# Kernel tuning notes

Hardware: AMD Instinct MI355X
Metric: run time of the kernel (lower is better)

## Reference

```python
import jax, jax.numpy as jnp
import numpy as np

N_HEADS = 16


def setup_inputs() -> dict:
    key = jax.random.key(0)
    ks = jax.random.split(key, 9)
    B, S, D = 2, 2048, 1024
    sc = 0.02
    return {
        'x': jax.random.normal(ks[0], (B, S, D), jnp.float32),
        'Wq': jax.random.normal(ks[1], (D, D), jnp.float32) * sc,
        'bq': jax.random.normal(ks[2], (D,), jnp.float32) * sc,
        'Wk': jax.random.normal(ks[3], (D, D), jnp.float32) * sc,
        'bk': jax.random.normal(ks[4], (D,), jnp.float32) * sc,
        'Wv': jax.random.normal(ks[5], (D, D), jnp.float32) * sc,
        'bv': jax.random.normal(ks[6], (D,), jnp.float32) * sc,
        'Wo': jax.random.normal(ks[7], (D, D), jnp.float32) * sc,
        'bo': jax.random.normal(ks[8], (D,), jnp.float32) * sc,
    }


def reference(x, Wq, bq, Wk, bk, Wv, bv, Wo, bo):
    # Chunked causal prefill. The chunk-wise mask (q_pos >= kv_pos over the
    # growing KV cache) is mathematically identical to full causal attention,
    # so we compute it as one vectorized masked softmax attention.
    B, S, D = x.shape
    H = N_HEADS
    hd = D // H

    def proj(W, b):
        # torch Linear: y = x @ W.T + b ; then split heads -> [B,H,S,hd]
        y = jnp.einsum('bsd,ed->bse', x, W) + b
        return y.reshape(B, S, H, hd).transpose(0, 2, 1, 3)

    q = proj(Wq, bq)
    k = proj(Wk, bk)
    v = proj(Wv, bv)

    scores = jnp.einsum('bhqd,bhkd->bhqk', q, k) / jnp.sqrt(jnp.asarray(hd, x.dtype))
    causal = jnp.tril(jnp.ones((S, S), dtype=bool))  # [S,S]
    scores = jnp.where(causal[None, None], scores, jnp.asarray(-jnp.inf, scores.dtype))
    attn = jax.nn.softmax(scores, axis=-1)
    ctx = jnp.einsum('bhqk,bhkd->bhqd', attn, v)  # [B,H,S,hd]
    ctx = ctx.transpose(0, 2, 1, 3).reshape(B, S, D)
    out = jnp.einsum('bsd,ed->bse', ctx, Wo) + bo
    return out
```

## Files before the change

### kernel.cpp

```cpp
#include <hip/hip_runtime.h>
#include <cstdint>
#include <math.h>

typedef _Float16 f16;
typedef _Float16 f16x2 __attribute__((ext_vector_type(2)));
typedef _Float16 f16x4 __attribute__((ext_vector_type(4)));
typedef _Float16 f16x8 __attribute__((ext_vector_type(8)));
typedef __fp16   h16x2 __attribute__((ext_vector_type(2)));
typedef float    f32x4 __attribute__((ext_vector_type(4)));

__device__ __forceinline__ f32x4 mfma16(f16x8 a, f16x8 b, f32x4 c) {
  return __builtin_amdgcn_mfma_f32_16x16x32_f16(a, b, c, 0, 0, 0);
}
__device__ __forceinline__ void gl2lds16(const f16* g, f16* l) {
  __builtin_amdgcn_global_load_lds((__attribute__((address_space(1))) void*)(g),
                                   (__attribute__((address_space(3))) void*)(l),
                                   16, 0, 0);
}
__device__ __forceinline__ float fexp2(float x) { return __builtin_amdgcn_exp2f(x); }
__device__ __forceinline__ f16x2 pkrtz(float a, float b) {
  h16x2 r = __builtin_amdgcn_cvt_pkrtz(a, b);
  return __builtin_bit_cast(f16x2, r);
}
__device__ __forceinline__ float dot2acc(f16x2 a, f16x2 b, float c) {
#if __has_builtin(__builtin_amdgcn_fdot2)
  return __builtin_amdgcn_fdot2(__builtin_bit_cast(h16x2, a),
                                __builtin_bit_cast(h16x2, b), c, false);
#else
  return c + (float)a[0] * (float)b[0] + (float)a[1] * (float)b[1];
#endif
}

__global__ __launch_bounds__(256) void cvt_kernel(
    const float* __restrict__ x,  const float* __restrict__ wq, const float* __restrict__ wk,
    const float* __restrict__ wv, const float* __restrict__ wo,
    f16* __restrict__ xh, f16* __restrict__ wqkvh, f16* __restrict__ woh)
{
  const int seg = blockIdx.y;
  const float* src; f16* dst; int n;
  if      (seg == 0) { src = x;  dst = xh;              n = 4194304; }
  else if (seg == 1) { src = wq; dst = wqkvh;           n = 1048576; }
  else if (seg == 2) { src = wk; dst = wqkvh + 1048576; n = 1048576; }
  else if (seg == 3) { src = wv; dst = wqkvh + 2097152; n = 1048576; }
  else               { src = wo; dst = woh;             n = 1048576; }
  const int idx = (int)(blockIdx.x * 256 + threadIdx.x) * 8;
  if (idx >= n) return;
  f32x4 a = *(const f32x4*)(src + idx);
  f32x4 b = *(const f32x4*)(src + idx + 4);
  f16x8 h;
  h[0] = (f16)a[0]; h[1] = (f16)a[1]; h[2] = (f16)a[2]; h[3] = (f16)a[3];
  h[4] = (f16)b[0]; h[5] = (f16)b[1]; h[6] = (f16)b[2]; h[7] = (f16)b[3];
  *(f16x8*)(dst + idx) = h;
}

__global__ __launch_bounds__(256) void gemm_qkv(
    const f16* __restrict__ A, const f16* __restrict__ B,
    const float* __restrict__ bias0, const float* __restrict__ bias1, const float* __restrict__ bias2,
    f16* __restrict__ Qp, f16* __restrict__ Kp, f16* __restrict__ Vp)
{
  constexpr int K = 1024;
  __shared__ __align__(16) f16 As[128 * 32];
  __shared__ __align__(16) f16 Bs[128 * 32];
  const int tid  = threadIdx.x;
  const int wave = tid >> 6, lane = tid & 63;
  const int quad = lane >> 4, col = lane & 15;
  const int tile_m = blockIdx.y * 128, tile_n = blockIdx.x * 128;
  const int mb = (wave >> 1) * 64, nb = (wave & 1) * 64;
  const int srow = lane >> 2, scol = (lane & 3) * 8;
  const f16* gA = A + (size_t)(tile_m + wave * 32 + srow) * K + scol;
  const f16* gB = B + (size_t)(tile_n + wave * 32 + srow) * K + scol;
  f16* lA = As + wave * 1024;
  f16* lB = Bs + wave * 1024;

  f32x4 acc[4][4] = {};
  for (int k0 = 0; k0 < K; k0 += 32) {
    gl2lds16(gA + k0,          lA);
    gl2lds16(gA + 16 * K + k0, lA + 512);
    gl2lds16(gB + k0,          lB);
    gl2lds16(gB + 16 * K + k0, lB + 512);
    __syncthreads();
    f16x8 af[4], bf[4];
    #pragma unroll
    for (int i = 0; i < 4; ++i)
      af[i] = *(const f16x8*)&As[(mb + i * 16 + col) * 32 + quad * 8];
    #pragma unroll
    for (int j = 0; j < 4; ++j)
      bf[j] = *(const f16x8*)&Bs[(nb + j * 16 + col) * 32 + quad * 8];
    #pragma unroll
    for (int i = 0; i < 4; ++i)
      #pragma unroll
      for (int j = 0; j < 4; ++j)
        acc[i][j] = mfma16(af[i], bf[j], acc[i][j]);
    __syncthreads();
  }

  #pragma unroll
  for (int j = 0; j < 4; ++j) {
    const int gn = tile_n + nb + j * 16 + col;
    const int which = gn >> 10;
    const int d = gn & 1023;
    const float* bp = (which == 0) ? bias0 : (which == 1) ? bias1 : bias2;
    f16* dst        = (which == 0) ? Qp    : (which == 1) ? Kp    : Vp;
    const float bvv = bp[d];
    const float qs  = (which == 0) ? 0.18033688f : 1.0f;
    const int h = d >> 6, hi = d & 63;
    #pragma unroll
    for (int i = 0; i < 4; ++i) {
      #pragma unroll
      for (int r = 0; r < 4; ++r) {
        const int gm = tile_m + mb + i * 16 + quad * 4 + r;
        const int bb = gm >> 11, s = gm & 2047;
        dst[(((size_t)bb * 16 + h) * 2048 + s) * 64 + hi] = (f16)((acc[i][j][r] + bvv) * qs);
      }
    }
  }
}

__global__ __launch_bounds__(256) void vtrans_kernel(
    const f16* __restrict__ Vh, f16* __restrict__ Vt)
{
  __shared__ __align__(16) f16 t[64][72];
  const int bh = blockIdx.y;
  const int s0 = blockIdx.x * 64;
  const int tid = threadIdx.x;
  const int sr = tid >> 2, dc = (tid & 3) * 16;
  const size_t ib = ((size_t)bh * 2048 + s0 + sr) * 64 + dc;
  f16x8 v0 = *(const f16x8*)&Vh[ib];
  f16x8 v1 = *(const f16x8*)&Vh[ib + 8];
  *(f16x8*)&t[sr][dc]     = v0;
  *(f16x8*)&t[sr][dc + 8] = v1;
  __syncthreads();
  const int d = tid >> 2, sc = (tid & 3) * 16;
  f16x8 o0, o1;
  #pragma unroll
  for (int j = 0; j < 8; ++j) { o0[j] = t[sc + j][d]; o1[j] = t[sc + 8 + j][d]; }
  const size_t ob = ((size_t)bh * 64 + d) * 2048 + s0 + sc;
  *(f16x8*)&Vt[ob]     = o0;
  *(f16x8*)&Vt[ob + 8] = o1;
}

__global__ __launch_bounds__(256) void attn_kernel(
    const f16* __restrict__ Q, const f16* __restrict__ K, const f16* __restrict__ Vt,
    f16* __restrict__ ctx)
{
  __shared__ __align__(16) f16 Ks[2][64 * 72];
  __shared__ __align__(16) f16 Vts[2][64 * 72];
  __shared__ __align__(16) f16 Ps[4][16 * 72];

  const int bh  = blockIdx.x;
  const int tid = threadIdx.x;
  const int wave = tid >> 6, lane = tid & 63;
  const int quad = lane >> 4, col = lane & 15;
  const int b = bh >> 4, h = bh & 15;
  const size_t base = (size_t)bh * 2048 * 64;
  const size_t vtb  = (size_t)bh * 64 * 2048;

  int srow[2], sc8[2];
  #pragma unroll
  for (int i = 0; i < 2; ++i) {
    const int flat = tid + i * 256;
    srow[i] = flat >> 3;
    sc8[i]  = (flat & 7) * 8;
  }

  auto run_tile = [&](int qt) {
    const int q0 = qt * 64;
    const int qa = q0 + wave * 16;
    const f16x8 bqa0 = *(const f16x8*)&Q[base + (size_t)(qa + col) * 64 + quad * 8];
    const f16x8 bqa1 = *(const f16x8*)&Q[base + (size_t)(qa + col) * 64 + 32 + quad * 8];

    f32x4 cta[4] = {};
    float ma = -INFINITY;
    float la = 0.f;

    f16x8 kr[2], vr[2];
    auto gload = [&](int t) {
      #pragma unroll
      for (int i = 0; i < 2; ++i) {
        kr[i] = *(const f16x8*)&K[base + (size_t)(t * 64 + srow[i]) * 64 + sc8[i]];
        vr[i] = *(const f16x8*)&Vt[vtb + (size_t)srow[i] * 2048 + t * 64 + sc8[i]];
      }
    };
    auto swrite = [&](int buf) {
      #pragma unroll
      for (int i = 0; i < 2; ++i) {
        *(f16x8*)&Ks[buf][srow[i] * 72 + sc8[i]]  = kr[i];
        *(f16x8*)&Vts[buf][srow[i] * 72 + sc8[i]] = vr[i];
      }
    };

    const int nIter = qt + 1;

    gload(0);
    __syncthreads();
    swrite(0);
    if (nIter > 1) gload(1);

    for (int t = 0; t < nIter; ++t) {
      const int cur = t & 1;
      __syncthreads();
      if (t + 1 < nIter) {
        swrite(cur ^ 1);
        if (t + 2 < nIter) gload(t + 2);
      }

      f32x4 sa[4];
      #pragma unroll
      for (int jt = 0; jt < 4; ++jt) {
        const int kro = (jt * 16 + col) * 72;
        const f16x8 ak0 = *(const f16x8*)&Ks[cur][kro + quad * 8];
        const f16x8 ak1 = *(const f16x8*)&Ks[cur][kro + 32 + quad * 8];
        f32x4 za = {};
        za = mfma16(ak0, bqa0, za);
        sa[jt] = mfma16(ak1, bqa1, za);
      }

      if (t == qt) {
        #pragma unroll
        for (int jt = 0; jt < 4; ++jt) {
          const int kg = t * 64 + jt * 16 + quad * 4;
          #pragma unroll
          for (int r = 0; r < 4; ++r) {
            if (kg + r > qa + col) sa[jt][r] = -1e30f;
          }
        }
      }

      float tm = fmaxf(fmaxf(sa[0][0], sa[0][1]), fmaxf(sa[0][2], sa[0][3]));
      #pragma unroll
      for (int jt = 1; jt < 4; ++jt)
        tm = fmaxf(tm, fmaxf(fmaxf(sa[jt][0], sa[jt][1]), fmaxf(sa[jt][2], sa[jt][3])));
      tm = fmaxf(tm, __shfl_xor(tm, 16));
      tm = fmaxf(tm, __shfl_xor(tm, 32));

      if (__any(tm > ma + 6.f)) {
        const float mnew = fmaxf(ma, tm);
        const float alpha = fexp2(ma - mnew);
        ma = mnew;
        la *= alpha;
        f32x4 ava;
        #pragma unroll
        for (int r = 0; r < 4; ++r) ava[r] = __shfl(alpha, quad * 4 + r);
        #pragma unroll
        for (int jd = 0; jd < 4; ++jd) cta[jd] *= ava;
      }

      const f16x2 one2 = {(_Float16)1.f, (_Float16)1.f};
      float rs = 0.f;
      #pragma unroll
      for (int jt = 0; jt < 4; ++jt) {
        const f16x2 a01 = pkrtz(fexp2(sa[jt][0] - ma), fexp2(sa[jt][1] - ma));
        const f16x2 a23 = pkrtz(fexp2(sa[jt][2] - ma), fexp2(sa[jt][3] - ma));
        rs = dot2acc(a01, one2, rs);
        rs = dot2acc(a23, one2, rs);
        f16x4 pw; pw[0] = a01[0]; pw[1] = a01[1]; pw[2] = a23[0]; pw[3] = a23[1];
        *(f16x4*)&Ps[wave][col * 72 + jt * 16 + quad * 4] = pw;
      }
      la += rs;

      __asm__ volatile("s_waitcnt lgkmcnt(0)" ::: "memory");

      const f16x8 apa0 = *(const f16x8*)&Ps[wave][col * 72 + quad * 8];
      const f16x8 apa1 = *(const f16x8*)&Ps[wave][col * 72 + 32 + quad * 8];
      #pragma unroll
      for (int jd = 0; jd < 4; ++jd) {
        const int vro = (jd * 16 + col) * 72;
        const f16x8 bv0 = *(const f16x8*)&Vts[cur][vro + quad * 8];
        const f16x8 bv1 = *(const f16x8*)&Vts[cur][vro + 32 + quad * 8];
        cta[jd] = mfma16(apa1, bv1, mfma16(apa0, bv0, cta[jd]));
      }
    }

    la += __shfl_xor(la, 16);
    la += __shfl_xor(la, 32);
    f32x4 lva;
    #pragma unroll
    for (int r = 0; r < 4; ++r) lva[r] = __shfl(la, quad * 4 + r);
    #pragma unroll
    for (int jd = 0; jd < 4; ++jd) {
      #pragma unroll
      for (int r = 0; r < 4; ++r) {
        const int qga = qa + quad * 4 + r;
        const int d = h * 64 + jd * 16 + col;
        ctx[((size_t)b * 2048 + qga) * 1024 + d] = (f16)(cta[jd][r] / lva[r]);
      }
    }
  };

  run_tile(blockIdx.y);
  run_tile(31 - blockIdx.y);
}

__global__ __launch_bounds__(256) void gemm_o(
    const f16* __restrict__ A, const f16* __restrict__ B, const float* __restrict__ bias,
    float* __restrict__ Out)
{
  constexpr int K = 1024;
  __shared__ __align__(16) f16 As[128 * 32];
  __shared__ __align__(16) f16 Bs[64 * 32];
  const int tid  = threadIdx.x;
  const int wave = tid >> 6, lane = tid & 63;
  const int quad = lane >> 4, col = lane & 15;
  const int tile_m = blockIdx.y * 128, tile_n = blockIdx.x * 64;
  const int mb = wave * 32;
  const int srow = lane >> 2, scol = (lane & 3) * 8;
  const f16* gA = A + (size_t)(tile_m + wave * 32 + srow) * K + scol;
  const f16* gB = B + (size_t)(tile_n + wave * 16 + srow) * K + scol;
  f16* lA = As + wave * 1024;
  f16* lB = Bs + wave * 512;

  f32x4 acc[2][4] = {};
  for (int k0 = 0; k0 < K; k0 += 32) {
    gl2lds16(gA + k0,          lA);
    gl2lds16(gA + 16 * K + k0, lA + 512);
    gl2lds16(gB + k0,          lB);
    __syncthreads();
    f16x8 af[2], bf[4];
    #pragma unroll
    for (int i = 0; i < 2; ++i)
      af[i] = *(const f16x8*)&As[(mb + i * 16 + col) * 32 + quad * 8];
    #pragma unroll
    for (int j = 0; j < 4; ++j)
      bf[j] = *(const f16x8*)&Bs[(j * 16 + col) * 32 + quad * 8];
    #pragma unroll
    for (int i = 0; i < 2; ++i)
      #pragma unroll
      for (int j = 0; j < 4; ++j)
        acc[i][j] = mfma16(af[i], bf[j], acc[i][j]);
    __syncthreads();
  }

  #pragma unroll
  for (int j = 0; j < 4; ++j) {
    const int gn = tile_n + j * 16 + col;
    const float bvv = bias[gn];
    #pragma unroll
    for (int i = 0; i < 2; ++i) {
      #pragma unroll
      for (int r = 0; r < 4; ++r) {
        const int gm = tile_m + mb + i * 16 + quad * 4 + r;
        Out[(size_t)gm * 1024 + gn] = acc[i][j][r] + bvv;
      }
    }
  }
}

extern "C" void kernel_launch(void* const* d_in, const int* in_sizes, int n_in,
                              void* d_out, int out_size, void* d_ws, size_t ws_size,
                              hipStream_t stream)
{
  const float* x  = (const float*)d_in[0];
  const float* Wq = (const float*)d_in[1];
  const float* bq = (const float*)d_in[2];
  const float* Wk = (const float*)d_in[3];
  const float* bk = (const float*)d_in[4];
  const float* Wv = (const float*)d_in[5];
  const float* bv = (const float*)d_in[6];
  const float* Wo = (const float*)d_in[7];
  const float* bo = (const float*)d_in[8];
  float* out = (float*)d_out;

  f16* ws = (f16*)d_ws;
  const size_t M1 = 1048576;
  f16* xh    = ws;
  f16* wqkvh = ws + 4  * M1;
  f16* woh   = ws + 7  * M1;
  f16* Qh    = ws + 8  * M1;
  f16* Kh    = ws + 12 * M1;
  f16* Vh    = ws + 16 * M1;
  f16* Vth   = ws + 20 * M1;
  f16* ctxh  = ws + 24 * M1;

  cvt_kernel<<<dim3(2048, 5), 256, 0, stream>>>(x, Wq, Wk, Wv, Wo, xh, wqkvh, woh);
  gemm_qkv<<<dim3(24, 32), 256, 0, stream>>>(xh, wqkvh, bq, bk, bv, Qh, Kh, Vh);
  vtrans_kernel<<<dim3(32, 32), 256, 0, stream>>>(Vh, Vth);
  attn_kernel<<<dim3(32, 16), 256, 0, stream>>>(Qh, Kh, Vth, ctxh);
  gemm_o<<<dim3(16, 32), 256, 0, stream>>>(ctxh, woh, bo, out);
}
```

Baseline: 191.6 us.

## Fuse paired causal query tiles into one KV sweep sharing K/V loads

Instead of running the short and long query tiles one after another, each block now streams KV tiles once for the long tile and also computes the short tile while its causal range is active. K/V tiles staged in shared memory are reused by both query tiles, which roughly halves global K/V traffic and barrier count per block. The blockIdx.y to tile-pair mapping is changed and occupancy is hinted with launch_bounds(256,4). The cost is more registers for two accumulator sets and a branchy loop body, which could limit occupancy or cause spills.

```diff
diff --git a/kernel.cpp b/kernel.cpp
--- a/kernel.cpp
+++ b/kernel.cpp
@@ -139,15 +139,18 @@
   *(f16x8*)&Vt[ob + 8] = o1;
 }
 
-__global__ __launch_bounds__(256) void attn_kernel(
+__global__ __launch_bounds__(256, 4) void attn_kernel(
     const f16* __restrict__ Q, const f16* __restrict__ K, const f16* __restrict__ Vt,
     f16* __restrict__ ctx)
 {
   __shared__ __align__(16) f16 Ks[2][64 * 72];
   __shared__ __align__(16) f16 Vts[2][64 * 72];
-  __shared__ __align__(16) f16 Ps[4][16 * 72];
+  __shared__ __align__(16) f16 Ps[4][2][16 * 72];
 
   const int bh  = blockIdx.x;
+  const int yy  = blockIdx.y;
+  const int p   = (yy < 8) ? yy : 23 - yy;
+  const int qlong = 31 - p, qshort = p;
   const int tid = threadIdx.x;
   const int wave = tid >> 6, lane = tid & 63;
   const int quad = lane >> 4, col = lane & 15;
@@ -163,76 +166,93 @@
     sc8[i]  = (flat & 7) * 8;
   }
 
-  auto run_tile = [&](int qt) {
-    const int q0 = qt * 64;
-    const int qa = q0 + wave * 16;
-    const f16x8 bqa0 = *(const f16x8*)&Q[base + (size_t)(qa + col) * 64 + quad * 8];
-    const f16x8 bqa1 = *(const f16x8*)&Q[base + (size_t)(qa + col) * 64 + 32 + quad * 8];
-
-    f32x4 cta[4] = {};
-    float ma = -INFINITY;
-    float la = 0.f;
-
-    f16x8 kr[2], vr[2];
-    auto gload = [&](int t) {
-      #pragma unroll
-      for (int i = 0; i < 2; ++i) {
-        kr[i] = *(const f16x8*)&K[base + (size_t)(t * 64 + srow[i]) * 64 + sc8[i]];
-        vr[i] = *(const f16x8*)&Vt[vtb + (size_t)srow[i] * 2048 + t * 64 + sc8[i]];
-      }
-    };
-    auto swrite = [&](int buf) {
-      #pragma unroll
-      for (int i = 0; i < 2; ++i) {
-        *(f16x8*)&Ks[buf][srow[i] * 72 + sc8[i]]  = kr[i];
-        *(f16x8*)&Vts[buf][srow[i] * 72 + sc8[i]] = vr[i];
-      }
-    };
-
-    const int nIter = qt + 1;
-
-    gload(0);
+  const int qa = qlong * 64 + wave * 16;
+  const int qb = qshort * 64 + wave * 16;
+  const f16x8 bqa0 = *(const f16x8*)&Q[base + (size_t)(qa + col) * 64 + quad * 8];
+  const f16x8 bqa1 = *(const f16x8*)&Q[base + (size_t)(qa + col) * 64 + 32 + quad * 8];
+  const f16x8 bqb0 = *(const f16x8*)&Q[base + (size_t)(qb + col) * 64 + quad * 8];
+  const f16x8 bqb1 = *(const f16x8*)&Q[base + (size_t)(qb + col) * 64 + 32 + quad * 8];
+
+  f32x4 cta[4] = {}, ctb[4] = {};
+  float ma = -INFINITY, la = 0.f;
+  float mb2 = -INFINITY, lb2 = 0.f;
+
+  f16x8 kr[2], vr[2];
+  auto gload = [&](int t) {
+    #pragma unroll
+    for (int i = 0; i < 2; ++i) {
+      kr[i] = *(const f16x8*)&K[base + (size_t)(t * 64 + srow[i]) * 64 + sc8[i]];
+      vr[i] = *(const f16x8*)&Vt[vtb + (size_t)srow[i] * 2048 + t * 64 + sc8[i]];
+    }
+  };
+  auto swrite = [&](int buf) {
+    #pragma unroll
+    for (int i = 0; i < 2; ++i) {
+      *(f16x8*)&Ks[buf][srow[i] * 72 + sc8[i]]  = kr[i];
+      *(f16x8*)&Vts[buf][srow[i] * 72 + sc8[i]] = vr[i];
+    }
+  };
+
+  const int nIter = qlong + 1;
+
+  gload(0);
+  __syncthreads();
+  swrite(0);
+  gload(1);
+
+  for (int t = 0; t < nIter; ++t) {
+    const int cur = t & 1;
     __syncthreads();
-    swrite(0);
-    if (nIter > 1) gload(1);
-
-    for (int t = 0; t < nIter; ++t) {
-      const int cur = t & 1;
-      __syncthreads();
-      if (t + 1 < nIter) {
-        swrite(cur ^ 1);
-        if (t + 2 < nIter) gload(t + 2);
-      }
-
-      f32x4 sa[4];
+    if (t + 1 < nIter) {
+      swrite(cur ^ 1);
+      if (t + 2 < nIter) gload(t + 2);
+    }
+    const bool doB = (t <= qshort);
+
+    f32x4 sa[4], sb[4];
+    #pragma unroll
+    for (int jt = 0; jt < 4; ++jt) {
+      const int kro = (jt * 16 + col) * 72;
+      const f16x8 ak0 = *(const f16x8*)&Ks[cur][kro + quad * 8];
+      const f16x8 ak1 = *(const f16x8*)&Ks[cur][kro + 32 + quad * 8];
+      f32x4 za = {};
+      za = mfma16(ak0, bqa0, za);
+      sa[jt] = mfma16(ak1, bqa1, za);
+      if (doB) {
+        f32x4 zb = {};
+        zb = mfma16(ak0, bqb0, zb);
+        sb[jt] = mfma16(ak1, bqb1, zb);
+      }
+    }
+
+    if (t == qlong) {
       #pragma unroll
       for (int jt = 0; jt < 4; ++jt) {
-        const int kro = (jt * 16 + col) * 72;
-        const f16x8 ak0 = *(const f16x8*)&Ks[cur][kro + quad * 8];
-        const f16x8 ak1 = *(const f16x8*)&Ks[cur][kro + 32 + quad * 8];
-        f32x4 za = {};
-        za = mfma16(ak0, bqa0, za);
-        sa[jt] = mfma16(ak1, bqa1, za);
-      }
-
-      if (t == qt) {
-        #pragma unroll
-        for (int jt = 0; jt < 4; ++jt) {
-          const int kg = t * 64 + jt * 16 + quad * 4;
-          #pragma unroll
-          for (int r = 0; r < 4; ++r) {
-            if (kg + r > qa + col) sa[jt][r] = -1e30f;
-          }
-        }
-      }
-
+        const int kg = t * 64 + jt * 16 + quad * 4;
+        #pragma unroll
+        for (int r = 0; r < 4; ++r)
+          if (kg + r > qa + col) sa[jt][r] = -1e30f;
+      }
+    }
+    if (t == qshort) {
+      #pragma unroll
+      for (int jt = 0; jt < 4; ++jt) {
+        const int kg = t * 64 + jt * 16 + quad * 4;
+        #pragma unroll
+        for (int r = 0; r < 4; ++r)
+          if (kg + r > qb + col) sb[jt][r] = -1e30f;
+      }
+    }
+
+    const f16x2 one2 = {(_Float16)1.f, (_Float16)1.f};
+
+    {
       float tm = fmaxf(fmaxf(sa[0][0], sa[0][1]), fmaxf(sa[0][2], sa[0][3]));
       #pragma unroll
       for (int jt = 1; jt < 4; ++jt)
         tm = fmaxf(tm, fmaxf(fmaxf(sa[jt][0], sa[jt][1]), fmaxf(sa[jt][2], sa[jt][3])));
       tm = fmaxf(tm, __shfl_xor(tm, 16));
       tm = fmaxf(tm, __shfl_xor(tm, 32));
-
       if (__any(tm > ma + 6.f)) {
         const float mnew = fmaxf(ma, tm);
         const float alpha = fexp2(ma - mnew);
@@ -244,8 +264,6 @@
         #pragma unroll
         for (int jd = 0; jd < 4; ++jd) cta[jd] *= ava;
       }
-
-      const f16x2 one2 = {(_Float16)1.f, (_Float16)1.f};
       float rs = 0.f;
       #pragma unroll
       for (int jt = 0; jt < 4; ++jt) {
@@ -254,23 +272,69 @@
         rs = dot2acc(a01, one2, rs);
         rs = dot2acc(a23, one2, rs);
         f16x4 pw; pw[0] = a01[0]; pw[1] = a01[1]; pw[2] = a23[0]; pw[3] = a23[1];
-        *(f16x4*)&Ps[wave][col * 72 + jt * 16 + quad * 4] = pw;
+        *(f16x4*)&Ps[wave][0][col * 72 + jt * 16 + quad * 4] = pw;
       }
       la += rs;
-
-      __asm__ volatile("s_waitcnt lgkmcnt(0)" ::: "memory");
-
-      const f16x8 apa0 = *(const f16x8*)&Ps[wave][col * 72 + quad * 8];
-      const f16x8 apa1 = *(const f16x8*)&Ps[wave][col * 72 + 32 + quad * 8];
+    }
+
+    if (doB) {
+      float tm = fmaxf(fmaxf(sb[0][0], sb[0][1]), fmaxf(sb[0][2], sb[0][3]));
+      #pragma unroll
+      for (int jt = 1; jt < 4; ++jt)
+        tm = fmaxf(tm, fmaxf(fmaxf(sb[jt][0], sb[jt][1]), fmaxf(sb[jt][2], sb[jt][3])));
+      tm = fmaxf(tm, __shfl_xor(tm, 16));
+      tm = fmaxf(tm, __shfl_xor(tm, 32));
+      if (__any(tm > mb2 + 6.f)) {
+        const float mnew = fmaxf(mb2, tm);
+        const float alpha = fexp2(mb2 - mnew);
+        mb2 = mnew;
+        lb2 *= alpha;
+        f32x4 avb;
+        #pragma unroll
+        for (int r = 0; r < 4; ++r) avb[r] = __shfl(alpha, quad * 4 + r);
+        #pragma unroll
+        for (int jd = 0; jd < 4; ++jd) ctb[jd] *= avb;
+      }
+      float rs = 0.f;
+      #pragma unroll
+      for (int jt = 0; jt < 4; ++jt) {
+        const f16x2 a01 = pkrtz(fexp2(sb[jt][0] - mb2), fexp2(sb[jt][1] - mb2));
+        const f16x2 a23 = pkrtz(fexp2(sb[jt][2] - mb2), fexp2(sb[jt][3] - mb2));
+        rs = dot2acc(a01, one2, rs);
+        rs = dot2acc(a23, one2, rs);
+        f16x4 pw; pw[0] = a01[0]; pw[1] = a01[1]; pw[2] = a23[0]; pw[3] = a23[1];
+        *(f16x4*)&Ps[wave][1][col * 72 + jt * 16 + quad * 4] = pw;
+      }
+      lb2 += rs;
+    }
+
+    __asm__ volatile("s_waitcnt lgkmcnt(0)" ::: "memory");
+
+    const f16x8 apa0 = *(const f16x8*)&Ps[wave][0][col * 72 + quad * 8];
+    const f16x8 apa1 = *(const f16x8*)&Ps[wave][0][col * 72 + 32 + quad * 8];
+    if (doB) {
+      const f16x8 apb0 = *(const f16x8*)&Ps[wave][1][col * 72 + quad * 8];
+      const f16x8 apb1 = *(const f16x8*)&Ps[wave][1][col * 72 + 32 + quad * 8];
       #pragma unroll
       for (int jd = 0; jd < 4; ++jd) {
         const int vro = (jd * 16 + col) * 72;
         const f16x8 bv0 = *(const f16x8*)&Vts[cur][vro + quad * 8];
         const f16x8 bv1 = *(const f16x8*)&Vts[cur][vro + 32 + quad * 8];
         cta[jd] = mfma16(apa1, bv1, mfma16(apa0, bv0, cta[jd]));
-      }
-    }
-
+        ctb[jd] = mfma16(apb1, bv1, mfma16(apb0, bv0, ctb[jd]));
+      }
+    } else {
+      #pragma unroll
+      for (int jd = 0; jd < 4; ++jd) {
+        const int vro = (jd * 16 + col) * 72;
+        const f16x8 bv0 = *(const f16x8*)&Vts[cur][vro + quad * 8];
+        const f16x8 bv1 = *(const f16x8*)&Vts[cur][vro + 32 + quad * 8];
+        cta[jd] = mfma16(apa1, bv1, mfma16(apa0, bv0, cta[jd]));
+      }
+    }
+  }
+
+  {
     la += __shfl_xor(la, 16);
     la += __shfl_xor(la, 32);
     f32x4 lva;
@@ -285,10 +349,23 @@
         ctx[((size_t)b * 2048 + qga) * 1024 + d] = (f16)(cta[jd][r] / lva[r]);
       }
     }
-  };
-
-  run_tile(blockIdx.y);
-  run_tile(31 - blockIdx.y);
+  }
+  {
+    lb2 += __shfl_xor(lb2, 16);
+    lb2 += __shfl_xor(lb2, 32);
+    f32x4 lvb;
+    #pragma unroll
+    for (int r = 0; r < 4; ++r) lvb[r] = __shfl(lb2, quad * 4 + r);
+    #pragma unroll
+    for (int jd = 0; jd < 4; ++jd) {
+      #pragma unroll
+      for (int r = 0; r < 4; ++r) {
+        const int qgb = qb + quad * 4 + r;
+        const int d = h * 64 + jd * 16 + col;
+        ctx[((size_t)b * 2048 + qgb) * 1024 + d] = (f16)(ctb[jd][r] / lvb[r]);
+      }
+    }
+  }
 }
 
 __global__ __launch_bounds__(256) void gemm_o(
```

New measurement: 193.5 us. No clear change (+1.0%).
